# Optimization experiments

Hardware: AMD Instinct MI355X
Metric: run time of the kernel (lower is better)

The kernel has to match this reference:

```python
import jax, jax.numpy as jnp
import numpy as np
import math

HEAD_NUM = 16
EPS = 1e-8


def modulated_linear(x, s, aff_w, aff_b, w, b):
    # x: [B,N,Fin], s: [B,S], aff_w: [Fin,S], w: [Fout,Fin]
    style = s @ aff_w.T + aff_b                      # [B,Fin]
    w_mod = w[None, :, :] * style[:, None, :]        # [B,Fout,Fin]
    demod = jax.lax.rsqrt(jnp.sum(w_mod * w_mod, axis=2) + EPS)  # [B,Fout]
    w_mod = w_mod * demod[:, :, None]
    return jnp.einsum('bni,boi->bno', x, w_mod) + b


def setup_inputs() -> dict:
    key = jax.random.key(0)
    ks = jax.random.split(key, 6)
    B, N, F, S = 8, 1024, 1024, 512
    return {
        'x': jax.random.normal(ks[0], (B, N, F), dtype=jnp.float32),
        's': jax.random.normal(ks[1], (B, S), dtype=jnp.float32),
        'k_aff_w': jax.random.normal(ks[2], (F, S), dtype=jnp.float32) * 0.02,
        'k_aff_b': jnp.ones((F,), dtype=jnp.float32),
        'k_w': jax.random.normal(ks[3], (F, F), dtype=jnp.float32) * 0.02,
        'k_b': jnp.zeros((F,), dtype=jnp.float32),
        'o_aff_w': jax.random.normal(ks[4], (F, S), dtype=jnp.float32) * 0.02,
        'o_aff_b': jnp.ones((F,), dtype=jnp.float32),
        'o_w': jax.random.normal(ks[5], (F, F), dtype=jnp.float32) * 0.02,
        'o_b': jnp.zeros((F,), dtype=jnp.float32),
    }


def reference(x, s, k_aff_w, k_aff_b, k_w, k_b, o_aff_w, o_aff_b, o_w, o_b):
    B, N, F = x.shape
    H = HEAD_NUM
    D = F // H
    # Source bug (kept faithful): q = k = v = k_mapping(x, s). Compute once.
    kx = modulated_linear(x, s, k_aff_w, k_aff_b, k_w, k_b)
    kx = kx.reshape(B, N, H, D)
    q = k = v = kx
    # Per-token head-mixing attention: HxH matrix per token (not NxN).
    scores = jnp.einsum('bnhd,bnjd->bnhj', q, k) / math.sqrt(D)
    A = jax.nn.softmax(scores, axis=-1)              # [B,N,H,H]
    out = jnp.einsum('bnhj,bnjd->bnhd', A, v).reshape(B, N, F)
    out = modulated_linear(out, s, o_aff_w, o_aff_b, o_w, o_b)
    return out
```

## Files before the change

kernel.cpp:

```cpp
#include <hip/hip_runtime.h>

typedef __attribute__((ext_vector_type(4))) float f32x4;
typedef __attribute__((ext_vector_type(8))) __bf16 bf16x8;
typedef __attribute__((ext_vector_type(8))) unsigned short ushort8;

__device__ __forceinline__ unsigned short f32_to_bf16(float f) {
  unsigned u = __builtin_bit_cast(unsigned, f);
  u += 0x7fffu + ((u >> 16) & 1u);
  return (unsigned short)(u >> 16);
}
__device__ __forceinline__ float wave_reduce_sum(float v) {
#pragma unroll
  for (int off = 32; off > 0; off >>= 1) v += __shfl_xor(v, off);
  return v;
}
__device__ __forceinline__ void gload_lds16(const void* g, void* l) {
  __builtin_amdgcn_global_load_lds(
      (const __attribute__((address_space(1))) unsigned int*)g,
      (__attribute__((address_space(3))) unsigned int*)l, 16, 0, 0);
}

__global__ void style_cast_kernel(const float* __restrict__ s,
                                  const float* __restrict__ kaw, const float* __restrict__ kab,
                                  const float* __restrict__ oaw, const float* __restrict__ oab,
                                  float* __restrict__ style_k, float* __restrict__ style_o,
                                  const float* __restrict__ x, unsigned short* __restrict__ xb) {
  if (blockIdx.x < 512) {
    const int gw = (int)((blockIdx.x * blockDim.x + threadIdx.x) >> 6);
    const int lane = threadIdx.x & 63;
    const int mat = gw >> 10;
    const int f = gw & 1023;
    const float4* awv = (const float4*)((mat ? oaw : kaw) + (size_t)f * 512 + lane * 8);
    const float4 a0 = awv[0], a1 = awv[1];
    const float bias = (mat ? oab : kab)[f];
    float* dst = (mat ? style_o : style_k);
#pragma unroll
    for (int b = 0; b < 8; ++b) {
      const float4* sv = (const float4*)(s + b * 512 + lane * 8);
      const float4 s0 = sv[0], s1 = sv[1];
      float acc = a0.x * s0.x + a0.y * s0.y + a0.z * s0.z + a0.w * s0.w +
                  a1.x * s1.x + a1.y * s1.y + a1.z * s1.z + a1.w * s1.w;
      acc = wave_reduce_sum(acc);
      if (lane == 0) dst[b * 1024 + f] = acc + bias;
    }
  } else {
    const size_t i = (size_t)(blockIdx.x - 512) * blockDim.x + threadIdx.x;
    const float4* src = (const float4*)x + i * 2;
    const float4 a = src[0];
    const float4 b4 = src[1];
    ushort8 w;
    w[0] = f32_to_bf16(a.x); w[1] = f32_to_bf16(a.y);
    w[2] = f32_to_bf16(a.z); w[3] = f32_to_bf16(a.w);
    w[4] = f32_to_bf16(b4.x); w[5] = f32_to_bf16(b4.y);
    w[6] = f32_to_bf16(b4.z); w[7] = f32_to_bf16(b4.w);
    ((ushort8*)xb)[i] = w;
  }
}

__global__ void modw_kernel(const float* __restrict__ kw, const float* __restrict__ ow,
                            const float* __restrict__ style_k, const float* __restrict__ style_o,
                            unsigned short* __restrict__ wmk, unsigned short* __restrict__ wmo) {
  const int gw = (int)((blockIdx.x * blockDim.x + threadIdx.x) >> 6);
  const int lane = threadIdx.x & 63;
  const int mat = gw >> 10;
  const int o = gw & 1023;
  const float4* wv = (const float4*)((mat ? ow : kw) + (size_t)o * 1024 + lane * 16);
  float w[16];
#pragma unroll
  for (int j = 0; j < 4; ++j) {
    const float4 t = wv[j];
    w[j * 4 + 0] = t.x; w[j * 4 + 1] = t.y; w[j * 4 + 2] = t.z; w[j * 4 + 3] = t.w;
  }
  const float* stb = mat ? style_o : style_k;
  unsigned short* wm = mat ? wmo : wmk;
#pragma unroll
  for (int b = 0; b < 8; ++b) {
    const float4* sv = (const float4*)(stb + b * 1024 + lane * 16);
    float v[16];
    float ss = 0.f;
#pragma unroll
    for (int j = 0; j < 4; ++j) {
      const float4 t = sv[j];
      v[j * 4 + 0] = w[j * 4 + 0] * t.x; v[j * 4 + 1] = w[j * 4 + 1] * t.y;
      v[j * 4 + 2] = w[j * 4 + 2] * t.z; v[j * 4 + 3] = w[j * 4 + 3] * t.w;
#pragma unroll
      for (int q = 0; q < 4; ++q) ss += v[j * 4 + q] * v[j * 4 + q];
    }
    ss = wave_reduce_sum(ss);
    const float demod = rsqrtf(ss + 1e-8f);
    ushort8 p0, p1;
#pragma unroll
    for (int t = 0; t < 8; ++t) {
      p0[t] = f32_to_bf16(v[t] * demod);
      p1[t] = f32_to_bf16(v[8 + t] * demod);
    }
    unsigned short* dst = wm + (((size_t)b << 10) + o) * 1024 + lane * 16;
    *(ushort8*)dst = p0;
    *(ushort8*)(dst + 8) = p1;
  }
}

template <bool OUT_BF16>
__launch_bounds__(512, 1)
__global__ void gemm_bt(const unsigned short* __restrict__ A,
                        const unsigned short* __restrict__ Bw,
                        const float* __restrict__ bias,
                        void* __restrict__ C) {
  constexpr int Kd = 1024;
  constexpr int NT = Kd / 64;
  __shared__ unsigned short As[2 * 128 * 64];
  __shared__ unsigned short Bs[2 * 256 * 64];
  const int id = blockIdx.x;
  const int bz = id & 7;
  const int chunk = id >> 3;
  const int tileN = (chunk & 3) << 8;
  const int tileM = (chunk >> 2) << 7;
  const int tid = threadIdx.x;
  const int wid = tid >> 6, lane = tid & 63;
  const int wr = wid >> 2, wc = wid & 3;
  const int frow = lane & 15, hi = lane >> 4;
  const unsigned short* Ab = A + ((size_t)bz * 1024 + tileM) * Kd;
  const unsigned short* Bb = Bw + ((size_t)bz * 1024 + tileN) * Kd;

  f32x4 acc[4][4];
#pragma unroll
  for (int m = 0; m < 4; ++m)
#pragma unroll
    for (int n = 0; n < 4; ++n) acc[m][n] = (f32x4){0.f, 0.f, 0.f, 0.f};

  const int wq = wid << 6;

  auto stage = [&](int buf, int kt) {
#pragma unroll
    for (int j = 0; j < 2; ++j) {
      const int qb = j * 512 + wq;
      const int q = qb + lane;
      const int r = q >> 3;
      const int sc = (q & 7) ^ (r & 7);
      gload_lds16(Ab + (size_t)r * Kd + kt * 64 + sc * 8, (void*)&As[buf * 8192 + qb * 8]);
    }
#pragma unroll
    for (int j = 0; j < 4; ++j) {
      const int qb = j * 512 + wq;
      const int q = qb + lane;
      const int r = q >> 3;
      const int sc = (q & 7) ^ (r & 7);
      gload_lds16(Bb + (size_t)r * Kd + kt * 64 + sc * 8, (void*)&Bs[buf * 16384 + qb * 8]);
    }
  };

  stage(0, 0);
  stage(1, 1);

  for (int kt = 0; kt < NT; ++kt) {
    const int buf = kt & 1;
    if (kt + 1 < NT) asm volatile("s_waitcnt vmcnt(6)" ::: "memory");
    else             asm volatile("s_waitcnt vmcnt(0)" ::: "memory");
    __builtin_amdgcn_s_barrier();
    asm volatile("" ::: "memory");

    bf16x8 av[4][2], bv[4][2];
#pragma unroll
    for (int m = 0; m < 4; ++m) {
      const int row = (wr << 6) + (m << 4) + frow;
#pragma unroll
      for (int ks = 0; ks < 2; ++ks) {
        const int ch = ((ks << 2) + hi) ^ (row & 7);
        av[m][ks] = *(const bf16x8*)&As[buf * 8192 + row * 64 + ch * 8];
      }
    }
#pragma unroll
    for (int n = 0; n < 4; ++n) {
      const int row = (wc << 6) + (n << 4) + frow;
#pragma unroll
      for (int ks = 0; ks < 2; ++ks) {
        const int ch = ((ks << 2) + hi) ^ (row & 7);
        bv[n][ks] = *(const bf16x8*)&Bs[buf * 16384 + row * 64 + ch * 8];
      }
    }
#pragma unroll
    for (int ks = 0; ks < 2; ++ks)
#pragma unroll
      for (int m = 0; m < 4; ++m)
#pragma unroll
        for (int n = 0; n < 4; ++n)
          acc[m][n] = __builtin_amdgcn_mfma_f32_16x16x32_bf16(av[m][ks], bv[n][ks],
                                                              acc[m][n], 0, 0, 0);
    asm volatile("s_waitcnt lgkmcnt(0)" ::: "memory");
    __builtin_amdgcn_s_barrier();
    asm volatile("" ::: "memory");
    if (kt + 2 < NT) stage(buf, kt + 2);
  }

  const int crow0 = tileM + (wr << 6);
  const int ccol0 = tileN + (wc << 6);
#pragma unroll
  for (int n = 0; n < 4; ++n) {
    const int col = ccol0 + n * 16 + frow;
    const float bias_c = bias[col];
#pragma unroll
    for (int m = 0; m < 4; ++m) {
#pragma unroll
      for (int i = 0; i < 4; ++i) {
        const int row = crow0 + m * 16 + (hi << 2) + i;
        const float v = acc[m][n][i] + bias_c;
        const size_t idx = ((size_t)bz * 1024 + row) * 1024 + col;
        if constexpr (OUT_BF16)
          ((unsigned short*)C)[idx] = f32_to_bf16(v);
        else
          ((float*)C)[idx] = v;
      }
    }
  }
}

__global__ void attn_kernel(const unsigned short* __restrict__ kx,
                            unsigned short* __restrict__ att) {
  __shared__ __align__(16) unsigned short KXl[4][16][72];
  __shared__ __align__(16) unsigned short Pl[4][16][24];
  const int w = threadIdx.x >> 6, lane = threadIdx.x & 63;
  const int token = (blockIdx.x << 2) + w;
  const int m = lane & 15, hi = lane >> 4;
  const unsigned short* src = kx + (size_t)token * 1024;

  ushort8 af0 = *(const ushort8*)(src + m * 64 + hi * 8);
  ushort8 af1 = *(const ushort8*)(src + m * 64 + 32 + hi * 8);
  *(ushort8*)&KXl[w][m][hi * 8] = af0;
  *(ushort8*)&KXl[w][m][32 + hi * 8] = af1;

  f32x4 s = {0.f, 0.f, 0.f, 0.f};
  s = __builtin_amdgcn_mfma_f32_16x16x32_bf16(__builtin_bit_cast(bf16x8, af0),
                                              __builtin_bit_cast(bf16x8, af0), s, 0, 0, 0);
  s = __builtin_amdgcn_mfma_f32_16x16x32_bf16(__builtin_bit_cast(bf16x8, af1),
                                              __builtin_bit_cast(bf16x8, af1), s, 0, 0, 0);
  float v[4], mx[4], sum[4];
#pragma unroll
  for (int i = 0; i < 4; ++i) { v[i] = s[i] * 0.125f; mx[i] = v[i]; }
#pragma unroll
  for (int off = 1; off <= 8; off <<= 1)
#pragma unroll
    for (int i = 0; i < 4; ++i) mx[i] = fmaxf(mx[i], __shfl_xor(mx[i], off));
#pragma unroll
  for (int i = 0; i < 4; ++i) { v[i] = __expf(v[i] - mx[i]); sum[i] = v[i]; }
#pragma unroll
  for (int off = 1; off <= 8; off <<= 1)
#pragma unroll
    for (int i = 0; i < 4; ++i) sum[i] += __shfl_xor(sum[i], off);
#pragma unroll
  for (int i = 0; i < 4; ++i) Pl[w][4 * hi + i][m] = f32_to_bf16(v[i] / sum[i]);

  asm volatile("s_waitcnt lgkmcnt(0)" ::: "memory");
  __builtin_amdgcn_sched_barrier(0);

  const int jb = (hi & 1) << 3;
  bf16x8 pa;
  if (hi < 2) pa = *(const bf16x8*)&Pl[w][m][jb];
  else        pa = (bf16x8){0, 0, 0, 0, 0, 0, 0, 0};
  unsigned short* dst = att + (size_t)token * 1024;
#pragma unroll
  for (int blk = 0; blk < 4; ++blk) {
    ushort8 bbu;
#pragma unroll
    for (int ii = 0; ii < 8; ++ii) bbu[ii] = KXl[w][jb + ii][blk * 16 + m];
    f32x4 o = {0.f, 0.f, 0.f, 0.f};
    o = __builtin_amdgcn_mfma_f32_16x16x32_bf16(pa, __builtin_bit_cast(bf16x8, bbu), o, 0, 0, 0);
#pragma unroll
    for (int i = 0; i < 4; ++i)
      dst[(4 * hi + i) * 64 + blk * 16 + m] = f32_to_bf16(o[i]);
  }
}

extern "C" void kernel_launch(void* const* d_in, const int* in_sizes, int n_in,
                              void* d_out, int out_size, void* d_ws, size_t ws_size,
                              hipStream_t stream) {
  const float* x     = (const float*)d_in[0];
  const float* s     = (const float*)d_in[1];
  const float* k_aff_w = (const float*)d_in[2];
  const float* k_aff_b = (const float*)d_in[3];
  const float* k_w   = (const float*)d_in[4];
  const float* k_b   = (const float*)d_in[5];
  const float* o_aff_w = (const float*)d_in[6];
  const float* o_aff_b = (const float*)d_in[7];
  const float* o_w   = (const float*)d_in[8];
  const float* o_b   = (const float*)d_in[9];
  float* out = (float*)d_out;

  char* ws = (char*)d_ws;
  float* style_k = (float*)(ws);
  float* style_o = (float*)(ws + (32 << 10));
  unsigned short* xb   = (unsigned short*)(ws + (64 << 10));
  unsigned short* wmk  = (unsigned short*)(ws + (64 << 10) + ((size_t)16 << 20));
  unsigned short* wmo  = (unsigned short*)(ws + (64 << 10) + ((size_t)32 << 20));
  unsigned short* kxb  = (unsigned short*)(ws + (64 << 10) + ((size_t)48 << 20));
  unsigned short* attb = (unsigned short*)(ws + (64 << 10) + ((size_t)64 << 20));

  style_cast_kernel<<<4608, 256, 0, stream>>>(s, k_aff_w, k_aff_b, o_aff_w, o_aff_b,
                                              style_k, style_o, x, xb);
  modw_kernel<<<512, 256, 0, stream>>>(k_w, o_w, style_k, style_o, wmk, wmo);
  gemm_bt<true><<<256, 512, 0, stream>>>(xb, wmk, k_b, (void*)kxb);
  attn_kernel<<<2048, 256, 0, stream>>>(kxb, attb);
  gemm_bt<false><<<256, 512, 0, stream>>>(attb, wmo, o_b, (void*)out);
}
```

Measured before the change: 82.40 us.

## Triple-buffer GEMM LDS tiles and drop the trailing per-iteration barrier

The GEMM moves from double to triple-buffered LDS staging. This lets the next-next tile load be issued mid-iteration into a third buffer, and the second barrier and lgkmcnt wait at the end of each k-step are removed. MFMA blocks are wrapped in s_setprio to favor math issue, and fragment loads are split into two halves around the global prefetch. LDS usage grows by half (to 144KB), which still fits at one block per CU. With vmcnt(6) unchanged, correctness depends on the three-buffer rotation keeping writes off the buffer being read.

```diff
diff --git a/kernel.cpp b/kernel.cpp
--- a/kernel.cpp
+++ b/kernel.cpp
@@ -108,8 +108,8 @@
                         void* __restrict__ C) {
   constexpr int Kd = 1024;
   constexpr int NT = Kd / 64;
-  __shared__ unsigned short As[2 * 128 * 64];
-  __shared__ unsigned short Bs[2 * 256 * 64];
+  __shared__ unsigned short As[3 * 128 * 64];
+  __shared__ unsigned short Bs[3 * 256 * 64];
   const int id = blockIdx.x;
   const int bz = id & 7;
   const int chunk = id >> 3;
@@ -152,44 +152,58 @@
   stage(0, 0);
   stage(1, 1);
 
+  int bufR = 0, bufW = 2;
   for (int kt = 0; kt < NT; ++kt) {
-    const int buf = kt & 1;
     if (kt + 1 < NT) asm volatile("s_waitcnt vmcnt(6)" ::: "memory");
     else             asm volatile("s_waitcnt vmcnt(0)" ::: "memory");
     __builtin_amdgcn_s_barrier();
     asm volatile("" ::: "memory");
 
+    const unsigned aOff = bufR * 8192, bOff = bufR * 16384;
     bf16x8 av[4][2], bv[4][2];
 #pragma unroll
     for (int m = 0; m < 4; ++m) {
       const int row = (wr << 6) + (m << 4) + frow;
-#pragma unroll
-      for (int ks = 0; ks < 2; ++ks) {
-        const int ch = ((ks << 2) + hi) ^ (row & 7);
-        av[m][ks] = *(const bf16x8*)&As[buf * 8192 + row * 64 + ch * 8];
-      }
+      const int ch = hi ^ (row & 7);
+      av[m][0] = *(const bf16x8*)&As[aOff + row * 64 + ch * 8];
     }
 #pragma unroll
     for (int n = 0; n < 4; ++n) {
       const int row = (wc << 6) + (n << 4) + frow;
-#pragma unroll
-      for (int ks = 0; ks < 2; ++ks) {
-        const int ch = ((ks << 2) + hi) ^ (row & 7);
-        bv[n][ks] = *(const bf16x8*)&Bs[buf * 16384 + row * 64 + ch * 8];
-      }
-    }
-#pragma unroll
-    for (int ks = 0; ks < 2; ++ks)
-#pragma unroll
-      for (int m = 0; m < 4; ++m)
-#pragma unroll
-        for (int n = 0; n < 4; ++n)
-          acc[m][n] = __builtin_amdgcn_mfma_f32_16x16x32_bf16(av[m][ks], bv[n][ks],
-                                                              acc[m][n], 0, 0, 0);
-    asm volatile("s_waitcnt lgkmcnt(0)" ::: "memory");
-    __builtin_amdgcn_s_barrier();
-    asm volatile("" ::: "memory");
-    if (kt + 2 < NT) stage(buf, kt + 2);
+      const int ch = hi ^ (row & 7);
+      bv[n][0] = *(const bf16x8*)&Bs[bOff + row * 64 + ch * 8];
+    }
+    if (kt + 2 < NT) stage(bufW, kt + 2);
+#pragma unroll
+    for (int m = 0; m < 4; ++m) {
+      const int row = (wr << 6) + (m << 4) + frow;
+      const int ch = (4 + hi) ^ (row & 7);
+      av[m][1] = *(const bf16x8*)&As[aOff + row * 64 + ch * 8];
+    }
+#pragma unroll
+    for (int n = 0; n < 4; ++n) {
+      const int row = (wc << 6) + (n << 4) + frow;
+      const int ch = (4 + hi) ^ (row & 7);
+      bv[n][1] = *(const bf16x8*)&Bs[bOff + row * 64 + ch * 8];
+    }
+    __builtin_amdgcn_s_setprio(1);
+#pragma unroll
+    for (int m = 0; m < 4; ++m)
+#pragma unroll
+      for (int n = 0; n < 4; ++n)
+        acc[m][n] = __builtin_amdgcn_mfma_f32_16x16x32_bf16(av[m][0], bv[n][0],
+                                                            acc[m][n], 0, 0, 0);
+    __builtin_amdgcn_s_setprio(0);
+    __builtin_amdgcn_s_setprio(1);
+#pragma unroll
+    for (int m = 0; m < 4; ++m)
+#pragma unroll
+      for (int n = 0; n < 4; ++n)
+        acc[m][n] = __builtin_amdgcn_mfma_f32_16x16x32_bf16(av[m][1], bv[n][1],
+                                                            acc[m][n], 0, 0, 0);
+    __builtin_amdgcn_s_setprio(0);
+    bufR = (bufR == 2) ? 0 : bufR + 1;
+    bufW = (bufW == 2) ? 0 : bufW + 1;
   }
 
   const int crow0 = tileM + (wr << 6);
```

Measured after the change: 85.29 us. 3.5% more time.

## Fold style modulation into activations and demod into GEMM epilogue, sharing unbatched weights

Applied to the files above, without the earlier changes.

Rewrites the modulated linear as (x*style) @ W^T * demod. The input style is applied while casting x to bf16, and the output style is applied in the attention kernel's store. Demodulation becomes a per-column scale in the GEMM epilogue, so the weights are cast to bf16 once and shared across the batch. This removes the per-batch modulated weight tensors (32 MB written and then re-read) in favour of small demod vectors, and the GEMM B operand now stays cache-resident across batches. The attention LDS layout is also transposed so B fragments load as vectors, which adds strided scalar LDS writes and changes bf16 rounding points.

```diff
diff --git a/kernel.cpp b/kernel.cpp
--- a/kernel.cpp
+++ b/kernel.cpp
@@ -20,83 +20,84 @@
       (__attribute__((address_space(3))) unsigned int*)l, 16, 0, 0);
 }
 
-__global__ void style_cast_kernel(const float* __restrict__ s,
-                                  const float* __restrict__ kaw, const float* __restrict__ kab,
-                                  const float* __restrict__ oaw, const float* __restrict__ oab,
-                                  float* __restrict__ style_k, float* __restrict__ style_o,
-                                  const float* __restrict__ x, unsigned short* __restrict__ xb) {
+__global__ void style_kernel(const float* __restrict__ s,
+                             const float* __restrict__ kaw, const float* __restrict__ kab,
+                             const float* __restrict__ oaw, const float* __restrict__ oab,
+                             float* __restrict__ style_k, float* __restrict__ style_o) {
+  const int gw = (int)((blockIdx.x * blockDim.x + threadIdx.x) >> 6);
+  const int lane = threadIdx.x & 63;
+  const int mat = gw >> 10;
+  const int f = gw & 1023;
+  const float4* awv = (const float4*)((mat ? oaw : kaw) + (size_t)f * 512 + lane * 8);
+  const float4 a0 = awv[0], a1 = awv[1];
+  const float bias = (mat ? oab : kab)[f];
+  float* dst = (mat ? style_o : style_k);
+#pragma unroll
+  for (int b = 0; b < 8; ++b) {
+    const float4* sv = (const float4*)(s + b * 512 + lane * 8);
+    const float4 s0 = sv[0], s1 = sv[1];
+    float acc = a0.x * s0.x + a0.y * s0.y + a0.z * s0.z + a0.w * s0.w +
+                a1.x * s1.x + a1.y * s1.y + a1.z * s1.z + a1.w * s1.w;
+    acc = wave_reduce_sum(acc);
+    if (lane == 0) dst[b * 1024 + f] = acc + bias;
+  }
+}
+
+__global__ void prep_kernel(const float* __restrict__ kw, const float* __restrict__ ow,
+                            const float* __restrict__ style_k, const float* __restrict__ style_o,
+                            float* __restrict__ dmk, float* __restrict__ dmo,
+                            unsigned short* __restrict__ wkb, unsigned short* __restrict__ wob,
+                            const float* __restrict__ x, unsigned short* __restrict__ xmod) {
   if (blockIdx.x < 512) {
     const int gw = (int)((blockIdx.x * blockDim.x + threadIdx.x) >> 6);
     const int lane = threadIdx.x & 63;
     const int mat = gw >> 10;
-    const int f = gw & 1023;
-    const float4* awv = (const float4*)((mat ? oaw : kaw) + (size_t)f * 512 + lane * 8);
-    const float4 a0 = awv[0], a1 = awv[1];
-    const float bias = (mat ? oab : kab)[f];
-    float* dst = (mat ? style_o : style_k);
+    const int o = gw & 1023;
+    const float* wrow = (mat ? ow : kw) + (size_t)o * 1024 + lane * 16;
+    float w[16];
+#pragma unroll
+    for (int j = 0; j < 4; ++j) {
+      const float4 t = ((const float4*)wrow)[j];
+      w[j * 4 + 0] = t.x; w[j * 4 + 1] = t.y; w[j * 4 + 2] = t.z; w[j * 4 + 3] = t.w;
+    }
+    const float* stb = mat ? style_o : style_k;
+    float* dm = mat ? dmo : dmk;
 #pragma unroll
     for (int b = 0; b < 8; ++b) {
-      const float4* sv = (const float4*)(s + b * 512 + lane * 8);
-      const float4 s0 = sv[0], s1 = sv[1];
-      float acc = a0.x * s0.x + a0.y * s0.y + a0.z * s0.z + a0.w * s0.w +
-                  a1.x * s1.x + a1.y * s1.y + a1.z * s1.z + a1.w * s1.w;
-      acc = wave_reduce_sum(acc);
-      if (lane == 0) dst[b * 1024 + f] = acc + bias;
-    }
+      const float4* sv = (const float4*)(stb + b * 1024 + lane * 16);
+      float ss = 0.f;
+#pragma unroll
+      for (int j = 0; j < 4; ++j) {
+        const float4 t = sv[j];
+        const float v0 = w[j * 4 + 0] * t.x, v1 = w[j * 4 + 1] * t.y;
+        const float v2 = w[j * 4 + 2] * t.z, v3 = w[j * 4 + 3] * t.w;
+        ss += v0 * v0 + v1 * v1 + v2 * v2 + v3 * v3;
+      }
+      ss = wave_reduce_sum(ss);
+      if (lane == 0) dm[b * 1024 + o] = rsqrtf(ss + 1e-8f);
+    }
+    unsigned short* wb = (mat ? wob : wkb) + (size_t)o * 1024 + lane * 16;
+    ushort8 p0, p1;
+#pragma unroll
+    for (int t = 0; t < 8; ++t) { p0[t] = f32_to_bf16(w[t]); p1[t] = f32_to_bf16(w[8 + t]); }
+    *(ushort8*)wb = p0;
+    *(ushort8*)(wb + 8) = p1;
   } else {
-    const size_t i = (size_t)(blockIdx.x - 512) * blockDim.x + threadIdx.x;
-    const float4* src = (const float4*)x + i * 2;
+    const size_t i8 = (size_t)(blockIdx.x - 512) * blockDim.x + threadIdx.x;
+    const size_t base = i8 * 8;
+    const int b = (int)(base >> 20);
+    const int i0 = (int)(base & 1023);
+    const float4* src = (const float4*)(x + base);
     const float4 a = src[0];
     const float4 b4 = src[1];
+    const float4* st = (const float4*)(style_k + b * 1024 + i0);
+    const float4 t0 = st[0], t1 = st[1];
     ushort8 w;
-    w[0] = f32_to_bf16(a.x); w[1] = f32_to_bf16(a.y);
-    w[2] = f32_to_bf16(a.z); w[3] = f32_to_bf16(a.w);
-    w[4] = f32_to_bf16(b4.x); w[5] = f32_to_bf16(b4.y);
-    w[6] = f32_to_bf16(b4.z); w[7] = f32_to_bf16(b4.w);
-    ((ushort8*)xb)[i] = w;
-  }
-}
-
-__global__ void modw_kernel(const float* __restrict__ kw, const float* __restrict__ ow,
-                            const float* __restrict__ style_k, const float* __restrict__ style_o,
-                            unsigned short* __restrict__ wmk, unsigned short* __restrict__ wmo) {
-  const int gw = (int)((blockIdx.x * blockDim.x + threadIdx.x) >> 6);
-  const int lane = threadIdx.x & 63;
-  const int mat = gw >> 10;
-  const int o = gw & 1023;
-  const float4* wv = (const float4*)((mat ? ow : kw) + (size_t)o * 1024 + lane * 16);
-  float w[16];
-#pragma unroll
-  for (int j = 0; j < 4; ++j) {
-    const float4 t = wv[j];
-    w[j * 4 + 0] = t.x; w[j * 4 + 1] = t.y; w[j * 4 + 2] = t.z; w[j * 4 + 3] = t.w;
-  }
-  const float* stb = mat ? style_o : style_k;
-  unsigned short* wm = mat ? wmo : wmk;
-#pragma unroll
-  for (int b = 0; b < 8; ++b) {
-    const float4* sv = (const float4*)(stb + b * 1024 + lane * 16);
-    float v[16];
-    float ss = 0.f;
-#pragma unroll
-    for (int j = 0; j < 4; ++j) {
-      const float4 t = sv[j];
-      v[j * 4 + 0] = w[j * 4 + 0] * t.x; v[j * 4 + 1] = w[j * 4 + 1] * t.y;
-      v[j * 4 + 2] = w[j * 4 + 2] * t.z; v[j * 4 + 3] = w[j * 4 + 3] * t.w;
-#pragma unroll
-      for (int q = 0; q < 4; ++q) ss += v[j * 4 + q] * v[j * 4 + q];
-    }
-    ss = wave_reduce_sum(ss);
-    const float demod = rsqrtf(ss + 1e-8f);
-    ushort8 p0, p1;
-#pragma unroll
-    for (int t = 0; t < 8; ++t) {
-      p0[t] = f32_to_bf16(v[t] * demod);
-      p1[t] = f32_to_bf16(v[8 + t] * demod);
-    }
-    unsigned short* dst = wm + (((size_t)b << 10) + o) * 1024 + lane * 16;
-    *(ushort8*)dst = p0;
-    *(ushort8*)(dst + 8) = p1;
+    w[0] = f32_to_bf16(a.x * t0.x); w[1] = f32_to_bf16(a.y * t0.y);
+    w[2] = f32_to_bf16(a.z * t0.z); w[3] = f32_to_bf16(a.w * t0.w);
+    w[4] = f32_to_bf16(b4.x * t1.x); w[5] = f32_to_bf16(b4.y * t1.y);
+    w[6] = f32_to_bf16(b4.z * t1.z); w[7] = f32_to_bf16(b4.w * t1.w);
+    ((ushort8*)xmod)[i8] = w;
   }
 }
 
@@ -104,6 +105,7 @@
 __launch_bounds__(512, 1)
 __global__ void gemm_bt(const unsigned short* __restrict__ A,
                         const unsigned short* __restrict__ Bw,
+                        const float* __restrict__ dm,
                         const float* __restrict__ bias,
                         void* __restrict__ C) {
   constexpr int Kd = 1024;
@@ -120,7 +122,7 @@
   const int wr = wid >> 2, wc = wid & 3;
   const int frow = lane & 15, hi = lane >> 4;
   const unsigned short* Ab = A + ((size_t)bz * 1024 + tileM) * Kd;
-  const unsigned short* Bb = Bw + ((size_t)bz * 1024 + tileN) * Kd;
+  const unsigned short* Bb = Bw + (size_t)tileN * Kd;
 
   f32x4 acc[4][4];
 #pragma unroll
@@ -197,13 +199,14 @@
 #pragma unroll
   for (int n = 0; n < 4; ++n) {
     const int col = ccol0 + n * 16 + frow;
+    const float dm_c = dm[bz * 1024 + col];
     const float bias_c = bias[col];
 #pragma unroll
     for (int m = 0; m < 4; ++m) {
 #pragma unroll
       for (int i = 0; i < 4; ++i) {
         const int row = crow0 + m * 16 + (hi << 2) + i;
-        const float v = acc[m][n][i] + bias_c;
+        const float v = acc[m][n][i] * dm_c + bias_c;
         const size_t idx = ((size_t)bz * 1024 + row) * 1024 + col;
         if constexpr (OUT_BF16)
           ((unsigned short*)C)[idx] = f32_to_bf16(v);
@@ -215,8 +218,9 @@
 }
 
 __global__ void attn_kernel(const unsigned short* __restrict__ kx,
+                            const float* __restrict__ style_o,
                             unsigned short* __restrict__ att) {
-  __shared__ __align__(16) unsigned short KXl[4][16][72];
+  __shared__ __align__(16) unsigned short KXt[4][64][17];
   __shared__ __align__(16) unsigned short Pl[4][16][24];
   const int w = threadIdx.x >> 6, lane = threadIdx.x & 63;
   const int token = (blockIdx.x << 2) + w;
@@ -225,8 +229,11 @@
 
   ushort8 af0 = *(const ushort8*)(src + m * 64 + hi * 8);
   ushort8 af1 = *(const ushort8*)(src + m * 64 + 32 + hi * 8);
-  *(ushort8*)&KXl[w][m][hi * 8] = af0;
-  *(ushort8*)&KXl[w][m][32 + hi * 8] = af1;
+#pragma unroll
+  for (int t = 0; t < 8; ++t) {
+    KXt[w][hi * 8 + t][m] = af0[t];
+    KXt[w][32 + hi * 8 + t][m] = af1[t];
+  }
 
   f32x4 s = {0.f, 0.f, 0.f, 0.f};
   s = __builtin_amdgcn_mfma_f32_16x16x32_bf16(__builtin_bit_cast(bf16x8, af0),
@@ -256,17 +263,18 @@
   bf16x8 pa;
   if (hi < 2) pa = *(const bf16x8*)&Pl[w][m][jb];
   else        pa = (bf16x8){0, 0, 0, 0, 0, 0, 0, 0};
+  const float* so = style_o + (size_t)(token >> 10) * 1024;
   unsigned short* dst = att + (size_t)token * 1024;
 #pragma unroll
   for (int blk = 0; blk < 4; ++blk) {
-    ushort8 bbu;
-#pragma unroll
-    for (int ii = 0; ii < 8; ++ii) bbu[ii] = KXl[w][jb + ii][blk * 16 + m];
+    const bf16x8 bb = *(const bf16x8*)&KXt[w][blk * 16 + m][jb];
     f32x4 o = {0.f, 0.f, 0.f, 0.f};
-    o = __builtin_amdgcn_mfma_f32_16x16x32_bf16(pa, __builtin_bit_cast(bf16x8, bbu), o, 0, 0, 0);
-#pragma unroll
-    for (int i = 0; i < 4; ++i)
-      dst[(4 * hi + i) * 64 + blk * 16 + m] = f32_to_bf16(o[i]);
+    o = __builtin_amdgcn_mfma_f32_16x16x32_bf16(pa, bb, o, 0, 0, 0);
+#pragma unroll
+    for (int i = 0; i < 4; ++i) {
+      const int f = (4 * hi + i) * 64 + blk * 16 + m;
+      dst[f] = f32_to_bf16(o[i] * so[f]);
+    }
   }
 }
 
@@ -288,16 +296,19 @@
   char* ws = (char*)d_ws;
   float* style_k = (float*)(ws);
   float* style_o = (float*)(ws + (32 << 10));
-  unsigned short* xb   = (unsigned short*)(ws + (64 << 10));
-  unsigned short* wmk  = (unsigned short*)(ws + (64 << 10) + ((size_t)16 << 20));
-  unsigned short* wmo  = (unsigned short*)(ws + (64 << 10) + ((size_t)32 << 20));
-  unsigned short* kxb  = (unsigned short*)(ws + (64 << 10) + ((size_t)48 << 20));
-  unsigned short* attb = (unsigned short*)(ws + (64 << 10) + ((size_t)64 << 20));
-
-  style_cast_kernel<<<4608, 256, 0, stream>>>(s, k_aff_w, k_aff_b, o_aff_w, o_aff_b,
-                                              style_k, style_o, x, xb);
-  modw_kernel<<<512, 256, 0, stream>>>(k_w, o_w, style_k, style_o, wmk, wmo);
-  gemm_bt<true><<<256, 512, 0, stream>>>(xb, wmk, k_b, (void*)kxb);
-  attn_kernel<<<2048, 256, 0, stream>>>(kxb, attb);
-  gemm_bt<false><<<256, 512, 0, stream>>>(attb, wmo, o_b, (void*)out);
-}
+  float* dmk     = (float*)(ws + (64 << 10));
+  float* dmo     = (float*)(ws + (96 << 10));
+  unsigned short* wkb  = (unsigned short*)(ws + ((size_t)1 << 20));
+  unsigned short* wob  = (unsigned short*)(ws + ((size_t)3 << 20));
+  unsigned short* xmod = (unsigned short*)(ws + ((size_t)8 << 20));
+  unsigned short* kxb  = (unsigned short*)(ws + ((size_t)24 << 20));
+  unsigned short* attb = (unsigned short*)(ws + ((size_t)40 << 20));
+
+  style_kernel<<<512, 256, 0, stream>>>(s, k_aff_w, k_aff_b, o_aff_w, o_aff_b,
+                                        style_k, style_o);
+  prep_kernel<<<4608, 256, 0, stream>>>(k_w, o_w, style_k, style_o,
+                                        dmk, dmo, wkb, wob, x, xmod);
+  gemm_bt<true><<<256, 512, 0, stream>>>(xmod, wkb, dmk, k_b, (void*)kxb);
+  attn_kernel<<<2048, 256, 0, stream>>>(kxb, style_o, attb);
+  gemm_bt<false><<<256, 512, 0, stream>>>(attb, wob, dmo, o_b, (void*)out);
+}
```

After: 81.33 us. No clear change (-1.3%).
